# Optimization experiments

Hardware: AMD Instinct MI355X
Metric: run time of the kernel (lower is better)

## Reference

```python
import jax, jax.numpy as jnp
import numpy as np
import math

D_MODEL = 1024
NHEAD = 16
SEQ_LEN = 4096
K_PROJ = 16
HEAD_DIM = D_MODEL // NHEAD


def setup_inputs() -> dict:
    key = jax.random.key(0)
    ks = jax.random.split(key, 11)
    x = jax.random.normal(ks[0], (4, SEQ_LEN, D_MODEL), dtype=jnp.float32)
    s = 1.0 / math.sqrt(D_MODEL)
    Wq = jax.random.uniform(ks[1], (D_MODEL, D_MODEL), minval=-s, maxval=s)
    bq = jax.random.uniform(ks[2], (D_MODEL,), minval=-s, maxval=s)
    Wk = jax.random.uniform(ks[3], (D_MODEL, D_MODEL), minval=-s, maxval=s)
    bk = jax.random.uniform(ks[4], (D_MODEL,), minval=-s, maxval=s)
    Wv = jax.random.uniform(ks[5], (D_MODEL, D_MODEL), minval=-s, maxval=s)
    bv = jax.random.uniform(ks[6], (D_MODEL,), minval=-s, maxval=s)
    Wo = jax.random.uniform(ks[7], (D_MODEL, D_MODEL), minval=-s, maxval=s)
    bo = jax.random.uniform(ks[8], (D_MODEL,), minval=-s, maxval=s)
    E = jax.random.normal(ks[9], (NHEAD, K_PROJ, SEQ_LEN)) * 0.02
    F = jax.random.normal(ks[10], (NHEAD, K_PROJ, SEQ_LEN)) * 0.02
    return {"x": x, "Wq": Wq, "bq": bq, "Wk": Wk, "bk": bk,
            "Wv": Wv, "bv": bv, "Wo": Wo, "bo": bo, "E": E, "F": F}


def reference(x, Wq, bq, Wk, bk, Wv, bv, Wo, bo, E, F):
    B, N, D = x.shape
    # torch Linear: y = x @ W.T + b
    q = x @ Wq.T + bq
    k = x @ Wk.T + bk
    v = x @ Wv.T + bv
    # [B, H, N, Dh]
    def split_heads(t):
        return t.reshape(B, N, NHEAD, HEAD_DIM).transpose(0, 2, 1, 3)
    q, k, v = split_heads(q), split_heads(k), split_heads(v)
    # low-rank projections of K, V along sequence: [B, H, Kp, Dh]
    k_lin = jnp.einsum('bhnd,hkn->bhkd', k, E)
    v_lin = jnp.einsum('bhnd,hkn->bhkd', v, F)
    scores = jnp.einsum('bhnd,bhkd->bhnk', q, k_lin) / math.sqrt(HEAD_DIM)
    attn = jax.nn.softmax(scores, axis=-1)  # dropout is identity in eval
    out = jnp.einsum('bhnk,bhkd->bhnd', attn, v_lin)
    out = out.transpose(0, 2, 1, 3).reshape(B, N, D)
    return out @ Wo.T + bo
```

## Files before the change

kernel.cpp:

```cpp
#include <hip/hip_runtime.h>
#include <hip/hip_bf16.h>

#define SEQLEN 4096

typedef __bf16 bf16x8 __attribute__((ext_vector_type(8)));
typedef float f32x4 __attribute__((ext_vector_type(4)));
typedef __attribute__((ext_vector_type(8))) unsigned short u16x8;

__device__ inline float bf2f(unsigned short s) {
  union { unsigned u; float f; } t; t.u = ((unsigned)s) << 16; return t.f;
}
__device__ inline unsigned short f2bf(float f) {
  __hip_bfloat16 h = __float2bfloat16(f);
  return *reinterpret_cast<unsigned short*>(&h);
}

__device__ inline void gload_lds16(const void* g, void* l) {
  __builtin_amdgcn_global_load_lds(
      (const __attribute__((address_space(1))) unsigned int*)g,
      (__attribute__((address_space(3))) unsigned int*)l, 16, 0, 0);
}

__global__ void cvt_f32_to_bf16(const float* __restrict__ s,
                                unsigned short* __restrict__ d, int n4) {
  int i = blockIdx.x * 256 + threadIdx.x;
  if (i >= n4) return;
  float4 v = reinterpret_cast<const float4*>(s)[i];
  ushort4 o;
  o.x = f2bf(v.x); o.y = f2bf(v.y); o.z = f2bf(v.z); o.w = f2bf(v.w);
  reinterpret_cast<ushort4*>(d)[i] = o;
}

__global__ void pack_bias(const float* __restrict__ a, const float* __restrict__ b,
                          const float* __restrict__ c, float* __restrict__ dst) {
  int i = blockIdx.x * 256 + threadIdx.x;
  if (i < 1024) { dst[i] = a[i]; dst[1024 + i] = b[i]; dst[2048 + i] = c[i]; }
}


#define MFMA16(mk, A00, A01, A10, A11)                                          \
  __builtin_amdgcn_s_setprio(1);                                                \
  _Pragma("unroll")                                                             \
  for (int n = 0; n < 4; ++n) {                                                 \
    acc[2*(mk)][n]   = __builtin_amdgcn_mfma_f32_16x16x32_bf16(A00, b[n][0], acc[2*(mk)][n],   0, 0, 0); \
    acc[2*(mk)][n]   = __builtin_amdgcn_mfma_f32_16x16x32_bf16(A01, b[n][1], acc[2*(mk)][n],   0, 0, 0); \
    acc[2*(mk)+1][n] = __builtin_amdgcn_mfma_f32_16x16x32_bf16(A10, b[n][0], acc[2*(mk)+1][n], 0, 0, 0); \
    acc[2*(mk)+1][n] = __builtin_amdgcn_mfma_f32_16x16x32_bf16(A11, b[n][1], acc[2*(mk)+1][n], 0, 0, 0); \
  }                                                                             \
  __builtin_amdgcn_s_setprio(0);

#define LDA8(mi, sg) (*reinterpret_cast<const bf16x8*>(&as[((wr << 7) + (mi) * 16 + r16) * 64 + (sg) * 8]))
#define LDB8(ni, sg) (*reinterpret_cast<const bf16x8*>(&bs[((wc << 6) + (ni) * 16 + r16) * 64 + (sg) * 8]))

template <typename OUT_T>
__global__ __launch_bounds__(512, 2) void gemm8p(
    const unsigned short* __restrict__ A, const unsigned short* __restrict__ B,
    const float* __restrict__ bias, OUT_T* __restrict__ C, int M, int N, int K,
    int ldc) {
  extern __shared__ __align__(16) unsigned short lds[];

  const int tid = threadIdx.x;
  const int lane = tid & 63, wv = tid >> 6;
  const int wr = wv >> 2, wc = wv & 3;
  const int r16 = lane & 15, kg = lane >> 4;
  const int sg0 = (0 * 4 + kg) ^ (r16 & 7);
  const int sg1 = (1 * 4 + kg) ^ (r16 & 7);

  const int nwg = gridDim.x;
  const int cpx = nwg >> 3;
  const int swz = ((int)blockIdx.x & 7) * cpx + ((int)blockIdx.x >> 3);
  const int mt = M >> 8;
  const int tile_m = swz % mt, tile_n = swz / mt;
  const int brow = tile_m << 8, bcol = tile_n << 8;

  const unsigned short* Ag = A + (size_t)brow * K;
  const unsigned short* Bg = B + (size_t)bcol * K;

  const int sr = tid >> 3;
  const int sc = tid & 7;
  const int sgl = sc ^ (sr & 7);

  auto STG = [&](const unsigned short* G, unsigned short* dstbuf, int row0, int kt) {
    gload_lds16(G + (size_t)(row0 + sr) * K + (size_t)kt * 64 + sgl * 8,
                dstbuf + (row0 + sr) * 64 + sc * 8);
  };

  f32x4 acc[8][4];
#pragma unroll
  for (int m = 0; m < 8; ++m)
#pragma unroll
    for (int n = 0; n < 4; ++n) acc[m][n] = (f32x4)0.0f;

  {
    unsigned short* a0 = lds;
    unsigned short* b0 = lds + 32768;
    STG(Ag, a0, 0, 0);   STG(Ag, a0, 128, 0);
    STG(Bg, b0, 0, 0);   STG(Bg, b0, 64, 0);
    STG(Bg, b0, 128, 0); STG(Bg, b0, 192, 0);
    STG(Ag, a0, 64, 0);  STG(Ag, a0, 192, 0);
  }
  asm volatile("s_waitcnt vmcnt(2)" ::: "memory");
  __builtin_amdgcn_s_barrier();

  const int NT = K >> 6;
  for (int t = 0; t < NT; ++t) {
    const int cur = t & 1;
    const unsigned short* as = lds + (cur << 14);
    const unsigned short* bs = lds + 32768 + (cur << 14);
    unsigned short* an = lds + ((cur ^ 1) << 14);
    unsigned short* bn = lds + 32768 + ((cur ^ 1) << 14);
    const int tn = (t + 1 < NT) ? t + 1 : 0;

    bf16x8 b[4][2];
#pragma unroll
    for (int n = 0; n < 4; ++n) { b[n][0] = LDB8(n, sg0); b[n][1] = LDB8(n, sg1); }

    {
      bf16x8 a00 = LDA8(0, sg0), a01 = LDA8(0, sg1);
      bf16x8 a10 = LDA8(1, sg0), a11 = LDA8(1, sg1);
      STG(Ag, an, 0, tn); STG(Ag, an, 128, tn);
      __builtin_amdgcn_s_barrier();
      MFMA16(0, a00, a01, a10, a11);
      __builtin_amdgcn_s_barrier();
    }
    {
      bf16x8 a00 = LDA8(2, sg0), a01 = LDA8(2, sg1);
      bf16x8 a10 = LDA8(3, sg0), a11 = LDA8(3, sg1);
      STG(Bg, bn, 0, tn); STG(Bg, bn, 64, tn);
      __builtin_amdgcn_s_barrier();
      MFMA16(1, a00, a01, a10, a11);
      asm volatile("s_waitcnt vmcnt(4)" ::: "memory");
      __builtin_amdgcn_s_barrier();
    }
    {
      bf16x8 a00 = LDA8(4, sg0), a01 = LDA8(4, sg1);
      bf16x8 a10 = LDA8(5, sg0), a11 = LDA8(5, sg1);
      STG(Bg, bn, 128, tn); STG(Bg, bn, 192, tn);
      __builtin_amdgcn_s_barrier();
      MFMA16(2, a00, a01, a10, a11);
      __builtin_amdgcn_s_barrier();
    }
    {
      bf16x8 a00 = LDA8(6, sg0), a01 = LDA8(6, sg1);
      bf16x8 a10 = LDA8(7, sg0), a11 = LDA8(7, sg1);
      STG(Ag, an, 64, tn); STG(Ag, an, 192, tn);
      __builtin_amdgcn_s_barrier();
      MFMA16(3, a00, a01, a10, a11);
      asm volatile("s_waitcnt vmcnt(2)" ::: "memory");
      __builtin_amdgcn_s_barrier();
    }
  }
  asm volatile("s_waitcnt vmcnt(0)" ::: "memory");

#pragma unroll
  for (int n = 0; n < 4; ++n) {
    int col = bcol + wc * 64 + n * 16 + r16;
    float bv = bias ? bias[col] : 0.0f;
#pragma unroll
    for (int m = 0; m < 8; ++m) {
#pragma unroll
      for (int r = 0; r < 4; ++r) {
        int row = brow + wr * 128 + m * 16 + kg * 4 + r;
        float v = acc[m][n][r] + bv;
        if constexpr (sizeof(OUT_T) == 2) {
          C[(size_t)row * ldc + col] = f2bf(v);
        } else {
          C[(size_t)row * ldc + col] = v;
        }
      }
    }
  }
}

__global__ void kvlin_part(const unsigned short* __restrict__ qkv,
                           const float* __restrict__ E, const float* __restrict__ F,
                           float* __restrict__ part) {
  __shared__ __align__(16) unsigned short Ks[128 * 64], Vs[128 * 64];
  __shared__ __align__(16) float Es[16 * 128], Fs[16 * 128];
  const int tid = threadIdx.x;
  const int bid = blockIdx.x;
  const int bh = bid >> 3, ns = bid & 7;
  const int b = bh >> 4, h = bh & 15;
  const int d = tid & 63, kk = tid >> 6;
  float aK[4] = {0, 0, 0, 0}, aV[4] = {0, 0, 0, 0};
  for (int c = 0; c < 4; ++c) {
    int n0 = ns * 512 + c * 128;
#pragma unroll
    for (int it = 0; it < 4; ++it) {
      int f = it * 256 + tid;
      int row = f >> 3, ch = f & 7;
      const unsigned short* gk =
          qkv + (size_t)(b * SEQLEN + n0 + row) * 3072 + 1024 + h * 64 + ch * 8;
      gload_lds16(gk, &Ks[f * 8]);
      gload_lds16(gk + 1024, &Vs[f * 8]);
    }
#pragma unroll
    for (int it = 0; it < 2; ++it) {
      int f = it * 256 + tid;
      int k = f >> 5, ch = f & 31;
      const float* ge = E + (size_t)(h * 16 + k) * SEQLEN + n0 + ch * 4;
      const float* gf = F + (size_t)(h * 16 + k) * SEQLEN + n0 + ch * 4;
      gload_lds16(ge, &Es[f * 4]);
      gload_lds16(gf, &Fs[f * 4]);
    }
    __syncthreads();
    for (int n = 0; n < 128; ++n) {
      float kv = bf2f(Ks[n * 64 + d]);
      float vv = bf2f(Vs[n * 64 + d]);
#pragma unroll
      for (int j = 0; j < 4; ++j) {
        aK[j] += Es[(kk * 4 + j) * 128 + n] * kv;
        aV[j] += Fs[(kk * 4 + j) * 128 + n] * vv;
      }
    }
    __syncthreads();
  }
  size_t base = ((size_t)ns * 64 + bh) * 2048;
#pragma unroll
  for (int j = 0; j < 4; ++j) {
    part[base + (kk * 4 + j) * 64 + d] = aK[j];
    part[base + 1024 + (kk * 4 + j) * 64 + d] = aV[j];
  }
}

__global__ void kvlin_reduce(const float* __restrict__ part, float* __restrict__ out) {
  int i = blockIdx.x * 256 + threadIdx.x;
  float s = 0;
#pragma unroll
  for (int ns = 0; ns < 8; ++ns) s += part[(size_t)ns * 131072 + i];
  out[i] = s;
}

__global__ void attn_kernel(const unsigned short* __restrict__ qkv,
                            const float* __restrict__ kvlin,
                            unsigned short* __restrict__ aout) {
  __shared__ float kl[1024], vl[1024];
  const int tid = threadIdx.x;
  const int bid = blockIdx.x;
  const int bh = bid >> 4, nt = bid & 15;
  const int b = bh >> 4, h = bh & 15;
  for (int i = tid; i < 1024; i += 256) {
    kl[i] = kvlin[(size_t)bh * 2048 + i];
    vl[i] = kvlin[(size_t)bh * 2048 + 1024 + i];
  }
  __syncthreads();
  const int n = nt * 256 + tid;
  const unsigned short* qp = qkv + (size_t)(b * SEQLEN + n) * 3072 + h * 64;
  float q[64];
#pragma unroll
  for (int c2 = 0; c2 < 8; ++c2) {
    u16x8 v = *reinterpret_cast<const u16x8*>(qp + c2 * 8);
#pragma unroll
    for (int j = 0; j < 8; ++j) q[c2 * 8 + j] = bf2f(v[j]);
  }
  float s[16];
#pragma unroll
  for (int k = 0; k < 16; ++k) {
    float a = 0;
#pragma unroll
    for (int dd = 0; dd < 64; ++dd) a += q[dd] * kl[k * 64 + dd];
    s[k] = a * 0.125f;
  }
  float mx = s[0];
#pragma unroll
  for (int k = 1; k < 16; ++k) mx = fmaxf(mx, s[k]);
  float sum = 0;
#pragma unroll
  for (int k = 0; k < 16; ++k) { s[k] = __expf(s[k] - mx); sum += s[k]; }
  float inv = 1.0f / sum;
#pragma unroll
  for (int k = 0; k < 16; ++k) s[k] *= inv;
  unsigned short* op = aout + (size_t)(b * SEQLEN + n) * 1024 + h * 64;
#pragma unroll
  for (int d0 = 0; d0 < 8; ++d0) {
    float o[8] = {0, 0, 0, 0, 0, 0, 0, 0};
#pragma unroll
    for (int k = 0; k < 16; ++k) {
      float p = s[k];
#pragma unroll
      for (int j = 0; j < 8; ++j) o[j] += p * vl[k * 64 + d0 * 8 + j];
    }
    u16x8 pk;
#pragma unroll
    for (int j = 0; j < 8; ++j) pk[j] = f2bf(o[j]);
    *reinterpret_cast<u16x8*>(op + d0 * 8) = pk;
  }
}

extern "C" void kernel_launch(void* const* d_in, const int* in_sizes, int n_in,
                              void* d_out, int out_size, void* d_ws, size_t ws_size,
                              hipStream_t stream) {
  const float* x  = (const float*)d_in[0];
  const float* Wq = (const float*)d_in[1];
  const float* bq = (const float*)d_in[2];
  const float* Wk = (const float*)d_in[3];
  const float* bk = (const float*)d_in[4];
  const float* Wv = (const float*)d_in[5];
  const float* bv = (const float*)d_in[6];
  const float* Wo = (const float*)d_in[7];
  const float* bo = (const float*)d_in[8];
  const float* E  = (const float*)d_in[9];
  const float* F  = (const float*)d_in[10];
  float* out = (float*)d_out;

  char* ws = (char*)d_ws;
  unsigned short* Xb   = (unsigned short*)(ws);
  unsigned short* Wqkv = (unsigned short*)(ws + 33554432);
  unsigned short* WoB  = (unsigned short*)(ws + 39845888);
  float*          Bqkv = (float*)(ws + 41943040);
  unsigned short* QKV  = (unsigned short*)(ws + 41955328);
  float*          KVp  = (float*)(ws + 142618624);
  float*          KVl  = (float*)(ws + 146812928);
  unsigned short* AOut = Xb;

  (void)hipFuncSetAttribute(reinterpret_cast<const void*>(gemm8p<unsigned short>),
                            hipFuncAttributeMaxDynamicSharedMemorySize, 131072);
  (void)hipFuncSetAttribute(reinterpret_cast<const void*>(gemm8p<float>),
                            hipFuncAttributeMaxDynamicSharedMemorySize, 131072);

  cvt_f32_to_bf16<<<16384, 256, 0, stream>>>(x, Xb, 4194304);
  cvt_f32_to_bf16<<<1024, 256, 0, stream>>>(Wq, Wqkv, 262144);
  cvt_f32_to_bf16<<<1024, 256, 0, stream>>>(Wk, Wqkv + 1048576, 262144);
  cvt_f32_to_bf16<<<1024, 256, 0, stream>>>(Wv, Wqkv + 2097152, 262144);
  cvt_f32_to_bf16<<<1024, 256, 0, stream>>>(Wo, WoB, 262144);
  pack_bias<<<4, 256, 0, stream>>>(bq, bk, bv, Bqkv);

  gemm8p<unsigned short><<<768, 512, 131072, stream>>>(
      Xb, Wqkv, Bqkv, QKV, 16384, 3072, 1024, 3072);

  kvlin_part<<<512, 256, 0, stream>>>(QKV, E, F, KVp);
  kvlin_reduce<<<512, 256, 0, stream>>>(KVp, KVl);
  attn_kernel<<<1024, 256, 0, stream>>>(QKV, KVl, AOut);

  gemm8p<float><<<256, 512, 131072, stream>>>(
      AOut, WoB, bo, out, 16384, 1024, 1024, 1024);
}
```

Before: 275.8 us.

## Prefetch B tile first and stage bf16 GEMM epilogue through swizzled LDS

Reorders the double-buffered global-to-LDS prefetch so the whole next B tile is issued in the first sub-step and the A tile afterwards, and adjusts the vmcnt wait thresholds to match. For bf16 outputs, the epilogue now writes bias-added results into XOR-swizzled LDS, then reads them back as 16-byte rows and stores them coalesced to global memory, replacing scattered 2-byte stores. This adds an extra barrier and LDS round-trip, and relies on the wait-count changes being correct for the new load order.

```diff
diff --git a/kernel.cpp b/kernel.cpp
--- a/kernel.cpp
+++ b/kernel.cpp
@@ -94,9 +94,9 @@
   {
     unsigned short* a0 = lds;
     unsigned short* b0 = lds + 32768;
-    STG(Ag, a0, 0, 0);   STG(Ag, a0, 128, 0);
     STG(Bg, b0, 0, 0);   STG(Bg, b0, 64, 0);
     STG(Bg, b0, 128, 0); STG(Bg, b0, 192, 0);
+    STG(Ag, a0, 0, 0);   STG(Ag, a0, 128, 0);
     STG(Ag, a0, 64, 0);  STG(Ag, a0, 192, 0);
   }
   asm volatile("s_waitcnt vmcnt(2)" ::: "memory");
@@ -118,7 +118,8 @@
     {
       bf16x8 a00 = LDA8(0, sg0), a01 = LDA8(0, sg1);
       bf16x8 a10 = LDA8(1, sg0), a11 = LDA8(1, sg1);
-      STG(Ag, an, 0, tn); STG(Ag, an, 128, tn);
+      STG(Bg, bn, 0, tn);   STG(Bg, bn, 64, tn);
+      STG(Bg, bn, 128, tn); STG(Bg, bn, 192, tn);
       __builtin_amdgcn_s_barrier();
       MFMA16(0, a00, a01, a10, a11);
       __builtin_amdgcn_s_barrier();
@@ -126,16 +127,16 @@
     {
       bf16x8 a00 = LDA8(2, sg0), a01 = LDA8(2, sg1);
       bf16x8 a10 = LDA8(3, sg0), a11 = LDA8(3, sg1);
-      STG(Bg, bn, 0, tn); STG(Bg, bn, 64, tn);
+      STG(Ag, an, 0, tn); STG(Ag, an, 128, tn);
       __builtin_amdgcn_s_barrier();
       MFMA16(1, a00, a01, a10, a11);
-      asm volatile("s_waitcnt vmcnt(4)" ::: "memory");
+      asm volatile("s_waitcnt vmcnt(6)" ::: "memory");
       __builtin_amdgcn_s_barrier();
     }
     {
       bf16x8 a00 = LDA8(4, sg0), a01 = LDA8(4, sg1);
       bf16x8 a10 = LDA8(5, sg0), a11 = LDA8(5, sg1);
-      STG(Bg, bn, 128, tn); STG(Bg, bn, 192, tn);
+      STG(Ag, an, 64, tn); STG(Ag, an, 192, tn);
       __builtin_amdgcn_s_barrier();
       MFMA16(2, a00, a01, a10, a11);
       __builtin_amdgcn_s_barrier();
@@ -143,7 +144,6 @@
     {
       bf16x8 a00 = LDA8(6, sg0), a01 = LDA8(6, sg1);
       bf16x8 a10 = LDA8(7, sg0), a11 = LDA8(7, sg1);
-      STG(Ag, an, 64, tn); STG(Ag, an, 192, tn);
       __builtin_amdgcn_s_barrier();
       MFMA16(3, a00, a01, a10, a11);
       asm volatile("s_waitcnt vmcnt(2)" ::: "memory");
@@ -152,20 +152,48 @@
   }
   asm volatile("s_waitcnt vmcnt(0)" ::: "memory");
 
-#pragma unroll
-  for (int n = 0; n < 4; ++n) {
-    int col = bcol + wc * 64 + n * 16 + r16;
-    float bv = bias ? bias[col] : 0.0f;
+  if constexpr (sizeof(OUT_T) == 2) {
+    __builtin_amdgcn_s_barrier();
+    unsigned short* C2 = reinterpret_cast<unsigned short*>(C);
+    float bvs[4];
+#pragma unroll
+    for (int n = 0; n < 4; ++n)
+      bvs[n] = bias ? bias[bcol + wc * 64 + n * 16 + r16] : 0.0f;
 #pragma unroll
     for (int m = 0; m < 8; ++m) {
 #pragma unroll
       for (int r = 0; r < 4; ++r) {
-        int row = brow + wr * 128 + m * 16 + kg * 4 + r;
-        float v = acc[m][n][r] + bv;
-        if constexpr (sizeof(OUT_T) == 2) {
-          C[(size_t)row * ldc + col] = f2bf(v);
-        } else {
-          C[(size_t)row * ldc + col] = v;
+        int rw = m * 16 + kg * 4 + r;
+        int xo = (rw & 12) << 2;
+#pragma unroll
+        for (int n = 0; n < 4; ++n) {
+          lds[wv * 8192 + rw * 64 + ((n * 16 + r16) ^ xo)] =
+              f2bf(acc[m][n][r] + bvs[n]);
+        }
+      }
+    }
+    __syncthreads();
+#pragma unroll
+    for (int p = 0; p < 16; ++p) {
+      int grow = p * 16 + (tid >> 5);
+      int g = tid & 31;
+      int wvs = ((grow >> 7) << 2) + (g >> 3);
+      int row_l = grow & 127;
+      int src = wvs * 8192 + row_l * 64 + (((g & 7) * 8) ^ ((row_l & 12) << 2));
+      u16x8 vv = *reinterpret_cast<const u16x8*>(&lds[src]);
+      *reinterpret_cast<u16x8*>(&C2[(size_t)(brow + grow) * ldc + bcol + g * 8]) = vv;
+    }
+  } else {
+#pragma unroll
+    for (int n = 0; n < 4; ++n) {
+      int col = bcol + wc * 64 + n * 16 + r16;
+      float bv = bias ? bias[col] : 0.0f;
+#pragma unroll
+      for (int m = 0; m < 8; ++m) {
+#pragma unroll
+        for (int r = 0; r < 4; ++r) {
+          int row = brow + wr * 128 + m * 16 + kg * 4 + r;
+          C[(size_t)row * ldc + col] = acc[m][n][r] + bv;
         }
       }
     }
```

Result: faster. 266.8 us (-3.3%).
